# Kernel optimization log

Hardware: AMD Instinct MI355X
Metric: run time of the kernel (lower is better)

Reference implementation:

```python
import jax, jax.numpy as jnp
import numpy as np

B, C, H, W = 4, 256, 64, 64


def setup_inputs() -> dict:
    key = jax.random.key(0)
    ks = jax.random.split(key, 8)
    s = 0.02
    return {
        "x": jax.random.normal(ks[0], (B, C, H, W), dtype=jnp.float32),
        "Wq": jax.random.normal(ks[1], (C, C), dtype=jnp.float32) * s,
        "bq": jax.random.normal(ks[2], (C,), dtype=jnp.float32) * s,
        "Wk": jax.random.normal(ks[3], (C, C), dtype=jnp.float32) * s,
        "bk": jax.random.normal(ks[4], (C,), dtype=jnp.float32) * s,
        "Wv": jax.random.normal(ks[5], (C, C), dtype=jnp.float32) * s,
        "bv": jax.random.normal(ks[6], (C,), dtype=jnp.float32) * s,
        "gamma": jax.random.normal(ks[7], (1,), dtype=jnp.float32),
    }


def reference(x, Wq, bq, Wk, bk, Wv, bv, gamma):
    b, c, h, w = x.shape
    n = h * w
    xf = x.reshape(b, c, n)  # [B,C,N]
    # 1x1 convs == per-pixel linear over channels
    q = jnp.einsum("oc,bcn->bon", Wq, xf) + bq[None, :, None]  # [B,C,N]
    k = jnp.einsum("oc,bcn->bon", Wk, xf) + bk[None, :, None]  # [B,C,N]
    v = jnp.einsum("oc,bcn->bon", Wv, xf) + bv[None, :, None]  # [B,C,N]
    # energy[b,i,j] = sum_c q[b,c,i] * k[b,c,j]  (Q^T K, no scale in original)
    energy = jnp.einsum("bci,bcj->bij", q, k)  # [B,N,N]
    attention = jax.nn.softmax(energy, axis=-1)  # softmax over j
    # out = V @ attention^T : out[b,c,i] = sum_j v[b,c,j] * attention[b,i,j]
    out = jnp.einsum("bcj,bij->bci", v, attention)  # [B,C,N]
    out = gamma[0] * out + xf
    return out.reshape(b, c, h, w)
```

## Files before the change

kernel.cpp:

```cpp
#include <hip/hip_runtime.h>
#include <hip/hip_bf16.h>

#define Bb 4
#define Cc 256
#define Nn 4096
#define NV 4160

typedef short s16x8 __attribute__((ext_vector_type(8)));
typedef float f32x4 __attribute__((ext_vector_type(4)));

__device__ __forceinline__ unsigned short f2bf(float f) {
    unsigned u = __builtin_bit_cast(unsigned, f);
    u += 0x7FFFu + ((u >> 16) & 1u);
    return (unsigned short)(u >> 16);
}

__device__ __forceinline__ unsigned pk2bf(float a, float b) {
    return (unsigned)f2bf(a) | ((unsigned)f2bf(b) << 16);
}

__device__ __forceinline__ f32x4 mfma16(s16x8 a, s16x8 b, f32x4 c) {
    return __builtin_amdgcn_mfma_f32_16x16x32_bf16(a, b, c, 0, 0, 0);
}

#if __has_builtin(__builtin_amdgcn_global_load_lds)
#define GL16(g, sdst)                                                              \
    __builtin_amdgcn_global_load_lds(                                              \
        (const __attribute__((address_space(1))) unsigned int*)(g),                \
        (__attribute__((address_space(3))) unsigned int*)(sdst), 16, 0, 0)
#else
#define GL16(g, sdst)                                                              \
    do {                                                                           \
        *(s16x8*)((char*)(sdst) + (threadIdx.x & 63) * 16) = *(const s16x8*)(g);   \
    } while (0)
#endif

__global__ void prep_w(const float* __restrict__ Wq, const float* __restrict__ Wk,
                       const float* __restrict__ Wv, unsigned short* __restrict__ Wbf) {
    int idx = (blockIdx.x * 256 + threadIdx.x) * 8;
    int mat = idx >> 16;
    int off = idx & 65535;
    const float* src = (mat == 0) ? Wq : ((mat == 1) ? Wk : Wv);
    float4 a = *(const float4*)(src + off);
    float4 b = *(const float4*)(src + off + 4);
    s16x8 o;
    o[0] = (short)f2bf(a.x); o[1] = (short)f2bf(a.y);
    o[2] = (short)f2bf(a.z); o[3] = (short)f2bf(a.w);
    o[4] = (short)f2bf(b.x); o[5] = (short)f2bf(b.y);
    o[6] = (short)f2bf(b.z); o[7] = (short)f2bf(b.w);
    *(s16x8*)(Wbf + idx) = o;
}

__global__ void transpose_x(const float* __restrict__ x, unsigned short* __restrict__ xT) {
    int b = blockIdx.z, c0 = blockIdx.y * 64, n0 = blockIdx.x * 64;
    __shared__ float tile[64][65];
    int t = threadIdx.x;
    int r = t >> 2, q = t & 3;
    const float* src = x + ((size_t)(b * Cc + c0 + r)) * Nn + n0 + q * 16;
#pragma unroll
    for (int j = 0; j < 4; j++) {
        float4 v4 = *(const float4*)(src + j * 4);
        tile[r][q * 16 + j * 4 + 0] = v4.x;
        tile[r][q * 16 + j * 4 + 1] = v4.y;
        tile[r][q * 16 + j * 4 + 2] = v4.z;
        tile[r][q * 16 + j * 4 + 3] = v4.w;
    }
    __syncthreads();
    unsigned short* dst = xT + ((size_t)b * Nn + n0 + r) * Cc + c0 + q * 16;
    s16x8 o0, o1;
#pragma unroll
    for (int j = 0; j < 8; j++) o0[j] = (short)f2bf(tile[q * 16 + j][r]);
#pragma unroll
    for (int j = 0; j < 8; j++) o1[j] = (short)f2bf(tile[q * 16 + 8 + j][r]);
    *(s16x8*)dst = o0;
    *(s16x8*)(dst + 8) = o1;
}

__global__ void proj(const unsigned short* __restrict__ xT, const unsigned short* __restrict__ Wbf,
                     const float* __restrict__ bq, const float* __restrict__ bk,
                     const float* __restrict__ bv,
                     unsigned short* __restrict__ qT, unsigned short* __restrict__ kT,
                     unsigned short* __restrict__ vO) {
    int nt0 = blockIdx.x * 64;
    int mat = blockIdx.y;
    int b   = blockIdx.z;
    int t = threadIdx.x, w = t >> 6, l = t & 63;
    int lr = l & 15, lg = l >> 4;
    const unsigned short* Wm  = Wbf + mat * (Cc * Cc);
    const float* bias = (mat == 0) ? bq : ((mat == 1) ? bk : bv);
    const unsigned short* xTb = xT + (size_t)b * Nn * Cc;

    if (mat < 2) {
        unsigned short* out = ((mat == 0) ? qT : kT) + (size_t)b * Nn * Cc;
        int nrow = nt0 + w * 16;
        s16x8 af[8];
#pragma unroll
        for (int kk = 0; kk < 8; kk++)
            af[kk] = *(const s16x8*)(xTb + (nrow + lr) * Cc + kk * 32 + lg * 8);
        for (int ct = 0; ct < 16; ct++) {
            f32x4 acca = {0, 0, 0, 0}, accb = {0, 0, 0, 0};
#pragma unroll
            for (int kk = 0; kk < 8; kk += 2) {
                s16x8 bfa = *(const s16x8*)(Wm + (ct * 16 + lr) * Cc + kk * 32 + lg * 8);
                s16x8 bfb = *(const s16x8*)(Wm + (ct * 16 + lr) * Cc + (kk + 1) * 32 + lg * 8);
                acca = mfma16(af[kk], bfa, acca);
                accb = mfma16(af[kk + 1], bfb, accb);
            }
            f32x4 acc = acca + accb;
            float bb = bias[ct * 16 + lr];
#pragma unroll
            for (int r = 0; r < 4; r++)
                out[(nrow + lg * 4 + r) * Cc + ct * 16 + lr] = f2bf(acc[r] + bb);
        }
    } else {
        unsigned short* out = vO + (size_t)b * Cc * NV;
        for (int mt = 0; mt < 4; mt++) {
            int crow = (w * 4 + mt) * 16;
            s16x8 af[8];
#pragma unroll
            for (int kk = 0; kk < 8; kk++)
                af[kk] = *(const s16x8*)(Wm + (crow + lr) * Cc + kk * 32 + lg * 8);
#pragma unroll
            for (int nt = 0; nt < 4; nt++) {
                f32x4 acca = {0, 0, 0, 0}, accb = {0, 0, 0, 0};
#pragma unroll
                for (int kk = 0; kk < 8; kk += 2) {
                    s16x8 bfa = *(const s16x8*)(xTb + (nt0 + nt * 16 + lr) * Cc + kk * 32 + lg * 8);
                    s16x8 bfb = *(const s16x8*)(xTb + (nt0 + nt * 16 + lr) * Cc + (kk + 1) * 32 + lg * 8);
                    acca = mfma16(af[kk], bfa, acca);
                    accb = mfma16(af[kk + 1], bfb, accb);
                }
                f32x4 acc = acca + accb;
#pragma unroll
                for (int r = 0; r < 4; r++) {
                    float bb = bias[crow + lg * 4 + r];
                    out[(size_t)(crow + lg * 4 + r) * NV + nt0 + nt * 16 + lr] = f2bf(acc[r] + bb);
                }
            }
        }
    }
}

__global__ void __launch_bounds__(256, 2)
attn(const unsigned short* __restrict__ qT, const unsigned short* __restrict__ kT,
     const unsigned short* __restrict__ vv,
     float* __restrict__ OPT, float* __restrict__ lp) {
    int id = blockIdx.x;
    int bs = id & 7, b = bs >> 1, s = bs & 1, iblk = id >> 3;
    int t = threadIdx.x, w = t >> 6, l = t & 63;
    int lr = l & 15, lg = l >> 4;
    int i0 = iblk * 64 + w * 16;

    __shared__ char Ks[2][16384];
    __shared__ char Vs[2][16384];

    const unsigned short* qb = qT + ((size_t)b * Nn + i0) * Cc;
    const char* kbase = (const char*)(kT + ((size_t)b * Nn + s * 2048) * Cc);
    const char* vbase = (const char*)(vv + (size_t)b * Cc * NV + s * 2048);

    s16x8 qf[8];
#pragma unroll
    for (int kk = 0; kk < 8; kk++)
        qf[kk] = *(const s16x8*)(qb + lr * Cc + kk * 32 + lg * 8);

    f32x4 O[16];
#pragma unroll
    for (int ct = 0; ct < 16; ct++) O[ct] = {0, 0, 0, 0};
    float lsum = 0.f;
    const float L2E = 1.44269504088896340736f;

#define STAGEK(bufi, jt)                                                        \
    {                                                                           \
        const char* ksl_ = kbase + (size_t)(jt) * 16384;                        \
        _Pragma("unroll") for (int i_ = 0; i_ < 4; i_++) {                      \
            int chunk_ = w * 4 + i_;                                            \
            int L_ = chunk_ * 1024 + l * 16;                                    \
            int row_ = L_ >> 9;                                                 \
            GL16(ksl_ + (L_ ^ ((row_ & 7) << 4)), &Ks[bufi][chunk_ * 1024]);    \
        }                                                                       \
    }

#define STAGEV(bufi, jt)                                                        \
    {                                                                           \
        _Pragma("unroll") for (int i_ = 0; i_ < 4; i_++) {                      \
            int chunk_ = w * 4 + i_;                                            \
            int row_ = chunk_ * 16 + (l >> 2);                                  \
            int colb_ = ((l & 3) * 16) ^ (((l >> 3) & 3) << 4);                 \
            GL16(vbase + (size_t)row_ * (NV * 2) + (size_t)(jt) * 64 + colb_,   \
                 &Vs[bufi][chunk_ * 1024]);                                     \
        }                                                                       \
    }

    STAGEK(0, 0);
    STAGEV(0, 0);
    asm volatile("s_waitcnt vmcnt(0)" ::: "memory");
    __syncthreads();
    int buf = 0;

    for (int jt = 0; jt < 64; jt++) {
        if (jt < 63) {
            STAGEK(buf ^ 1, jt + 1);
            STAGEV(buf ^ 1, jt + 1);
        }
        const char* ksb = Ks[buf];
        f32x4 E0 = {0, 0, 0, 0}, E1 = {0, 0, 0, 0};
        __builtin_amdgcn_s_setprio(1);
#pragma unroll
        for (int kk = 0; kk < 8; kk++) {
            int cb = (kk * 64 + lg * 16) ^ ((lr & 7) << 4);
            s16x8 k0 = *(const s16x8*)(ksb + lr * 512 + cb);
            s16x8 k1 = *(const s16x8*)(ksb + (16 + lr) * 512 + cb);
            E0 = mfma16(k0, qf[kk], E0);
            E1 = mfma16(k1, qf[kk], E1);
        }
        __builtin_amdgcn_s_setprio(0);
        const char* vsb = Vs[buf];
        int vswz = (lg * 16) ^ (((lr >> 1) & 3) << 4);
        s16x8 vfr[16];
#pragma unroll
        for (int ct = 0; ct < 16; ct++)
            vfr[ct] = *(const s16x8*)(vsb + (ct * 16 + lr) * 64 + vswz);
        float p0[4], p1[4];
#pragma unroll
        for (int r = 0; r < 4; r++) {
            p0[r] = exp2f(E0[r] * L2E);
            p1[r] = exp2f(E1[r] * L2E);
            lsum += p0[r] + p1[r];
        }
        unsigned h0a = pk2bf(p0[0], p0[1]), h0b = pk2bf(p0[2], p0[3]);
        unsigned h1a = pk2bf(p1[0], p1[1]), h1b = pk2bf(p1[2], p1[3]);
        int sA = lr + ((lg & 1) << 5);
        int sB = sA + 16;
        unsigned a0 = (unsigned)__shfl((int)h0a, sA);
        unsigned b0 = (unsigned)__shfl((int)h1a, sA);
        unsigned a1 = (unsigned)__shfl((int)h0b, sA);
        unsigned b1 = (unsigned)__shfl((int)h1b, sA);
        unsigned a2 = (unsigned)__shfl((int)h0a, sB);
        unsigned b2 = (unsigned)__shfl((int)h1a, sB);
        unsigned a3 = (unsigned)__shfl((int)h0b, sB);
        unsigned b3 = (unsigned)__shfl((int)h1b, sB);
        bool losel = (lg < 2);
        uint4 pw;
        pw.x = losel ? a0 : b0;
        pw.y = losel ? a1 : b1;
        pw.z = losel ? a2 : b2;
        pw.w = losel ? a3 : b3;
        s16x8 pf = __builtin_bit_cast(s16x8, pw);
        __builtin_amdgcn_s_setprio(1);
#pragma unroll
        for (int ct = 0; ct < 16; ct++)
            O[ct] = mfma16(vfr[ct], pf, O[ct]);
        __builtin_amdgcn_s_setprio(0);
        asm volatile("s_waitcnt vmcnt(0)" ::: "memory");
        __syncthreads();
        buf ^= 1;
    }

    lsum += __shfl_xor(lsum, 16);
    lsum += __shfl_xor(lsum, 32);
    size_t sb = (size_t)(s * Bb + b);
    if (lg == 0)
        lp[sb * Nn + i0 + lr] = lsum;
    float* ob = OPT + sb * Nn * Cc;
#pragma unroll
    for (int ct = 0; ct < 16; ct++)
        *(f32x4*)(ob + (size_t)(i0 + lr) * Cc + ct * 16 + lg * 4) = O[ct];
#undef STAGEK
#undef STAGEV
}

__global__ void __launch_bounds__(256)
merge(const float* __restrict__ OPT, const float* __restrict__ lp,
      const float* __restrict__ x, const float* __restrict__ gamma,
      float* __restrict__ out) {
    int b = blockIdx.z, c0 = blockIdx.y * 64, n0 = blockIdx.x * 64;
    __shared__ float tile[64][65];
    __shared__ float linv[64];
    int t = threadIdx.x;
    if (t < 64) {
        float sum = lp[(size_t)b * Nn + n0 + t] + lp[(size_t)(Bb + b) * Nn + n0 + t];
        linv[t] = 1.0f / sum;
    }
    __syncthreads();
    float g = gamma[0];
    int r = t >> 2, q = t & 3;
    const float* p0 = OPT + ((size_t)b * Nn + n0 + r) * Cc + c0 + q * 16;
    const float* p1 = OPT + ((size_t)(Bb + b) * Nn + n0 + r) * Cc + c0 + q * 16;
    float sc = g * linv[r];
#pragma unroll
    for (int j = 0; j < 4; j++) {
        float4 a0 = *(const float4*)(p0 + j * 4);
        float4 a1 = *(const float4*)(p1 + j * 4);
        tile[r][q * 16 + j * 4 + 0] = sc * (a0.x + a1.x);
        tile[r][q * 16 + j * 4 + 1] = sc * (a0.y + a1.y);
        tile[r][q * 16 + j * 4 + 2] = sc * (a0.z + a1.z);
        tile[r][q * 16 + j * 4 + 3] = sc * (a0.w + a1.w);
    }
    __syncthreads();
    const float* xp = x + ((size_t)b * Cc + c0 + r) * Nn + n0 + q * 16;
    float* op = out + ((size_t)b * Cc + c0 + r) * Nn + n0 + q * 16;
#pragma unroll
    for (int j = 0; j < 4; j++) {
        float4 xv = *(const float4*)(xp + j * 4);
        float4 o4;
        o4.x = tile[q * 16 + j * 4 + 0][r] + xv.x;
        o4.y = tile[q * 16 + j * 4 + 1][r] + xv.y;
        o4.z = tile[q * 16 + j * 4 + 2][r] + xv.z;
        o4.w = tile[q * 16 + j * 4 + 3][r] + xv.w;
        *(float4*)(op + j * 4) = o4;
    }
}

extern "C" void kernel_launch(void* const* d_in, const int* in_sizes, int n_in,
                              void* d_out, int out_size, void* d_ws, size_t ws_size,
                              hipStream_t stream) {
    (void)in_sizes; (void)n_in; (void)out_size; (void)ws_size;
    const float* x     = (const float*)d_in[0];
    const float* Wq    = (const float*)d_in[1];
    const float* bq    = (const float*)d_in[2];
    const float* Wk    = (const float*)d_in[3];
    const float* bk    = (const float*)d_in[4];
    const float* Wv    = (const float*)d_in[5];
    const float* bv    = (const float*)d_in[6];
    const float* gamma = (const float*)d_in[7];
    float* out = (float*)d_out;

    const size_t XTN = (size_t)Bb * Nn * Cc;
    const size_t VSZ = (size_t)Bb * Cc * NV;
    unsigned short* xT  = (unsigned short*)d_ws;
    unsigned short* Wbf = xT + XTN;
    unsigned short* qT  = Wbf + 3 * Cc * Cc;
    unsigned short* kT  = qT + XTN;
    unsigned short* vv  = kT + XTN;
    float*          OPT = (float*)(vv + VSZ);
    float*          lp  = OPT + 2 * XTN;

    hipLaunchKernelGGL(prep_w, dim3(96), dim3(256), 0, stream, Wq, Wk, Wv, Wbf);
    hipLaunchKernelGGL(transpose_x, dim3(Nn / 64, Cc / 64, Bb), dim3(256), 0, stream, x, xT);
    hipLaunchKernelGGL(proj, dim3(Nn / 64, 3, Bb), dim3(256), 0, stream,
                       xT, Wbf, bq, bk, bv, qT, kT, vv);
    hipLaunchKernelGGL(attn, dim3(512), dim3(256), 0, stream,
                       qT, kT, vv, OPT, lp);
    hipLaunchKernelGGL(merge, dim3(Nn / 64, Cc / 64, Bb), dim3(256), 0, stream,
                       OPT, lp, x, gamma, out);
}
```

Before: 186.5 us.

## Software-pipeline QK^T one tile ahead of softmax and PV in attention loop

```diff
diff --git a/kernel.cpp b/kernel.cpp
--- a/kernel.cpp
+++ b/kernel.cpp
@@ -191,30 +191,34 @@
         }                                                                       \
     }
 
+#define QKT(e0, e1, bufi)                                                       \
+    {                                                                           \
+        const char* ksb_ = Ks[bufi];                                            \
+        __builtin_amdgcn_s_setprio(1);                                          \
+        _Pragma("unroll") for (int kk = 0; kk < 8; kk++) {                      \
+            int cb_ = (kk * 64 + lg * 16) ^ ((lr & 7) << 4);                    \
+            s16x8 k0_ = *(const s16x8*)(ksb_ + lr * 512 + cb_);                 \
+            s16x8 k1_ = *(const s16x8*)(ksb_ + (16 + lr) * 512 + cb_);          \
+            e0 = mfma16(k0_, qf[kk], e0);                                       \
+            e1 = mfma16(k1_, qf[kk], e1);                                       \
+        }                                                                       \
+        __builtin_amdgcn_s_setprio(0);                                          \
+    }
+
     STAGEK(0, 0);
     STAGEV(0, 0);
+    STAGEK(1, 1);
     asm volatile("s_waitcnt vmcnt(0)" ::: "memory");
     __syncthreads();
-    int buf = 0;
+    f32x4 E0 = {0, 0, 0, 0}, E1 = {0, 0, 0, 0};
+    QKT(E0, E1, 0);
 
     for (int jt = 0; jt < 64; jt++) {
-        if (jt < 63) {
-            STAGEK(buf ^ 1, jt + 1);
-            STAGEV(buf ^ 1, jt + 1);
-        }
-        const char* ksb = Ks[buf];
-        f32x4 E0 = {0, 0, 0, 0}, E1 = {0, 0, 0, 0};
-        __builtin_amdgcn_s_setprio(1);
-#pragma unroll
-        for (int kk = 0; kk < 8; kk++) {
-            int cb = (kk * 64 + lg * 16) ^ ((lr & 7) << 4);
-            s16x8 k0 = *(const s16x8*)(ksb + lr * 512 + cb);
-            s16x8 k1 = *(const s16x8*)(ksb + (16 + lr) * 512 + cb);
-            E0 = mfma16(k0, qf[kk], E0);
-            E1 = mfma16(k1, qf[kk], E1);
-        }
-        __builtin_amdgcn_s_setprio(0);
-        const char* vsb = Vs[buf];
+        if (jt <= 61) STAGEK(jt & 1, jt + 2);
+        if (jt <= 62) STAGEV((jt + 1) & 1, jt + 1);
+        f32x4 En0 = {0, 0, 0, 0}, En1 = {0, 0, 0, 0};
+        QKT(En0, En1, (jt + 1) & 1);
+        const char* vsb = Vs[jt & 1];
         int vswz = (lg * 16) ^ (((lr >> 1) & 3) << 4);
         s16x8 vfr[16];
 #pragma unroll
@@ -251,9 +255,9 @@
         for (int ct = 0; ct < 16; ct++)
             O[ct] = mfma16(vfr[ct], pf, O[ct]);
         __builtin_amdgcn_s_setprio(0);
-        asm volatile("s_waitcnt vmcnt(0)" ::: "memory");
-        __syncthreads();
-        buf ^= 1;
+        if (jt < 63) __syncthreads();
+        E0 = En0;
+        E1 = En1;
     }
 
     lsum += __shfl_xor(lsum, 16);
@@ -267,6 +271,7 @@
         *(f32x4*)(ob + (size_t)(i0 + lr) * Cc + ct * 16 + lg * 4) = O[ct];
 #undef STAGEK
 #undef STAGEV
+#undef QKT
 }
 
 __global__ void __launch_bounds__(256)
```

After: 188.8 us. No clear change (+1.3%).
